# Performance work log

Hardware: AMD Instinct MI355X
Metric: run time of the kernel (lower is better)

## Reference

```python
import jax, jax.numpy as jnp
import numpy as np

N = 100000
E = 1600000
D_IN = 128
D_HID = 128
D_OUT = 64


def setup_inputs() -> dict:
    key = jax.random.key(0)
    ks = jax.random.split(key, 12)
    x = jax.random.normal(ks[0], (N, D_IN), dtype=jnp.float32)
    src = jax.random.randint(ks[1], (E,), 0, N, dtype=jnp.int32)
    dst = jax.random.randint(ks[2], (E,), 0, N, dtype=jnp.int32)
    def lin(k, din, dout):
        s = 1.0 / np.sqrt(din)
        return jax.random.uniform(k, (din, dout), jnp.float32, -s, s)
    return {
        "x": x, "src": src, "dst": dst,
        "Ws0": lin(ks[3], D_IN, D_HID), "Wn0": lin(ks[4], D_IN, D_HID), "b0": jnp.zeros((D_HID,), jnp.float32),
        "Ws1": lin(ks[5], D_HID, D_HID), "Wn1": lin(ks[6], D_HID, D_HID), "b1": jnp.zeros((D_HID,), jnp.float32),
        "Ws2": lin(ks[7], D_HID, D_OUT), "Wn2": lin(ks[8], D_HID, D_OUT), "b2": jnp.zeros((D_OUT,), jnp.float32),
    }


def _sage_conv(h, src, dst, Ws, Wn, b):
    # mean aggregation of neighbor (src) features onto dst nodes
    deg = jax.ops.segment_sum(jnp.ones((src.shape[0],), h.dtype), dst, num_segments=N)
    agg = jax.ops.segment_sum(h[src], dst, num_segments=N)  # [N, d_in]
    mean = agg / jnp.maximum(deg, 1.0)[:, None]
    return h @ Ws + mean @ Wn + b


def reference(x, src, dst, Ws0, Wn0, b0, Ws1, Wn1, b1, Ws2, Wn2, b2):
    h = _sage_conv(x, src, dst, Ws0, Wn0, b0)
    h = jax.nn.relu(h)  # dropout is identity in eval mode
    h = _sage_conv(h, src, dst, Ws1, Wn1, b1)
    h = jax.nn.relu(h)
    h = _sage_conv(h, src, dst, Ws2, Wn2, b2)
    return h
```

## Files before the change

### kernel.cpp

```cpp
#include <hip/hip_runtime.h>

#define NN 100000
#define NE 1600000
#define DF 128
#define TS 136
#define NCB 391
#define NWA 256
#define SZA 6250
#define NH (NCB * NWA)
#define CAPB 6144

typedef unsigned int uint32;
typedef unsigned short u16;
typedef _Float16 f16;
typedef f16 f16x8 __attribute__((ext_vector_type(8)));
typedef f16 f16x2 __attribute__((ext_vector_type(2)));
typedef float f32x4 __attribute__((ext_vector_type(4)));

__device__ __forceinline__ uint32 pk2(float a, float b) {
    union { f16x2 h; uint32 u; } v;
    v.h.x = (f16)a; v.h.y = (f16)b;
    return v.u;
}
__device__ __forceinline__ u16 f2h(float a) {
    union { f16 h; u16 u; } v; v.h = (f16)a; return v.u;
}


__global__ __launch_bounds__(256) void histA(const int* __restrict__ dst,
                                             int* __restrict__ H) {
    __shared__ int lh[NCB];
    int w = blockIdx.x, t = threadIdx.x;
    for (int i = t; i < NCB; i += 256) lh[i] = 0;
    __syncthreads();
    int e0 = w * SZA, e1 = min(e0 + SZA, NE);
    for (int e = e0 + t; e < e1; e += 256) atomicAdd(&lh[dst[e] >> 8], 1);
    __syncthreads();
    for (int i = t; i < NCB; i += 256) H[i * NWA + w] = lh[i];
}

__global__ __launch_bounds__(256) void sumCB(const int* __restrict__ H,
                                             int* __restrict__ CBT) {
    __shared__ int sm[256];
    int cb = blockIdx.x, t = threadIdx.x;
    sm[t] = H[cb * NWA + t];
    __syncthreads();
    for (int off = 128; off > 0; off >>= 1) {
        if (t < off) sm[t] += sm[t + off];
        __syncthreads();
    }
    if (t == 0) CBT[cb] = sm[0];
}

__global__ __launch_bounds__(512) void scanCBW(const int* __restrict__ CBT,
                                               const int* __restrict__ H,
                                               int* __restrict__ O,
                                               int* __restrict__ rowptr) {
    __shared__ int sm[512];
    __shared__ int sh[256];
    int cb = blockIdx.x, t = threadIdx.x;
    int v = (t < NCB) ? CBT[t] : 0;
    sm[t] = v;
    __syncthreads();
    for (int off = 1; off < 512; off <<= 1) {
        int x = (t >= off) ? sm[t - off] : 0;
        __syncthreads();
        sm[t] += x;
        __syncthreads();
    }
    if (cb == 0 && t == NCB - 1) {
        O[NH] = sm[t];
        rowptr[NN] = sm[t];
    }
    int cbo = sm[cb] - CBT[cb];
    int hv = (t < 256) ? H[cb * NWA + t] : 0;
    if (t < 256) sh[t] = hv;
    __syncthreads();
    for (int off = 1; off < 256; off <<= 1) {
        int x = (t >= off && t < 256) ? sh[t - off] : 0;
        __syncthreads();
        if (t < 256) sh[t] += x;
        __syncthreads();
    }
    if (t < 256) O[cb * NWA + t] = cbo + sh[t] - hv;
}

__global__ __launch_bounds__(1024) void passA(const int* __restrict__ src,
                                              const int* __restrict__ dst,
                                              const int* __restrict__ O,
                                              uint32* __restrict__ ebuf) {
    __shared__ int cur[NCB];
    int w = blockIdx.x, t = threadIdx.x;
    for (int i = t; i < NCB; i += 1024) cur[i] = O[i * NWA + w];
    __syncthreads();
    int e0 = w * SZA, e1 = min(e0 + SZA, NE);
    for (int e = e0 + t; e < e1; e += 1024) {
        int d = dst[e];
        int cb = d >> 8;
        int p = atomicAdd(&cur[cb], 1);
        ebuf[p] = ((uint32)src[e] << 8) | (uint32)(d & 255);
    }
}

__global__ __launch_bounds__(256) void passB(const uint32* __restrict__ ebuf,
                                             const int* __restrict__ O,
                                             int* __restrict__ rowptr,
                                             int* __restrict__ col) {
    __shared__ int hist[256], start[256], cur[256];
    __shared__ int seg[CAPB];
    int cb = blockIdx.x, t = threadIdx.x;
    int base = O[cb * NWA], end = O[(cb + 1) * NWA];
    int m = end - base;
    hist[t] = 0;
    __syncthreads();
    for (int i = t; i < m; i += 256) atomicAdd(&hist[ebuf[base + i] & 255], 1);
    __syncthreads();
    int v = hist[t];
    cur[t] = v;
    __syncthreads();
    for (int off = 1; off < 256; off <<= 1) {
        int x = (t >= off) ? cur[t - off] : 0;
        __syncthreads();
        cur[t] += x;
        __syncthreads();
    }
    start[t] = cur[t] - v;
    __syncthreads();
    int node = cb * 256 + t;
    if (node < NN) rowptr[node] = base + start[t];
    cur[t] = start[t];
    __syncthreads();
    if (m <= CAPB) {
        for (int i = t; i < m; i += 256) {
            uint32 u = ebuf[base + i];
            int p = atomicAdd(&cur[u & 255], 1);
            seg[p] = (int)(u >> 8);
        }
        __syncthreads();
        for (int i = t; i < m; i += 256) col[base + i] = seg[i];
    } else {
        for (int i = t; i < m; i += 256) {
            uint32 u = ebuf[base + i];
            int p = atomicAdd(&cur[u & 255], 1);
            col[base + p] = (int)(u >> 8);
        }
    }
}

__global__ void prep_cvt(const float* __restrict__ Ws0, const float* __restrict__ Wn0,
                         const float* __restrict__ Ws1, const float* __restrict__ Wn1,
                         const float* __restrict__ Ws2, const float* __restrict__ Wn2,
                         u16* __restrict__ WB,
                         const float* __restrict__ x, uint2* __restrict__ xh) {
    int b = blockIdx.x;
    if (b < 320) {
        int t = b * 256 + threadIdx.x;
        if (t < 65536) {
            int m = t >> 14;
            int local = t & 16383;
            int k = local >> 7, n = local & 127;
            const float* W = (m == 0) ? Ws0 : (m == 1) ? Wn0 : (m == 2) ? Ws1 : Wn1;
            WB[m * 16384 + n * 128 + k] = f2h(W[k * 128 + n]);
        } else {
            int local = t - 65536;
            int half = local >> 13;
            int idx = local & 8191;
            int k = idx >> 6, n = idx & 63;
            const float* W = half ? Wn2 : Ws2;
            WB[4 * 16384 + (n + half * 64) * 128 + k] = f2h(W[k * 64 + n]);
        }
    } else {
        int t = (b - 320) * 256 + threadIdx.x;
        if (t < NN * DF / 4) {
            float4 v = ((const float4*)x)[t];
            uint2 o;
            o.x = pk2(v.x, v.y);
            o.y = pk2(v.z, v.w);
            xh[t] = o;
        }
    }
}

__global__ __launch_bounds__(256) void gather_add_f16(const u16* __restrict__ gb,
                                                      const int* __restrict__ rowptr,
                                                      const int* __restrict__ col,
                                                      float* __restrict__ out) {
    int node = blockIdx.x * 32 + (threadIdx.x >> 3);
    int g = threadIdx.x & 7;
    int s = rowptr[node], e = rowptr[node + 1];
    float acc[8];
#pragma unroll
    for (int i = 0; i < 8; ++i) acc[i] = 0.f;
    int j = s;
    for (; j + 7 < e; j += 8) {
        int n0 = col[j],     n1 = col[j + 1], n2 = col[j + 2], n3 = col[j + 3];
        int n4 = col[j + 4], n5 = col[j + 5], n6 = col[j + 6], n7 = col[j + 7];
        f16x8 v0 = *(const f16x8*)(gb + (size_t)n0 * 64 + g * 8);
        f16x8 v1 = *(const f16x8*)(gb + (size_t)n1 * 64 + g * 8);
        f16x8 v2 = *(const f16x8*)(gb + (size_t)n2 * 64 + g * 8);
        f16x8 v3 = *(const f16x8*)(gb + (size_t)n3 * 64 + g * 8);
        f16x8 v4 = *(const f16x8*)(gb + (size_t)n4 * 64 + g * 8);
        f16x8 v5 = *(const f16x8*)(gb + (size_t)n5 * 64 + g * 8);
        f16x8 v6 = *(const f16x8*)(gb + (size_t)n6 * 64 + g * 8);
        f16x8 v7 = *(const f16x8*)(gb + (size_t)n7 * 64 + g * 8);
        f16x8 sA = (v0 + v1) + (v2 + v3);
        f16x8 sB = (v4 + v5) + (v6 + v7);
#pragma unroll
        for (int i = 0; i < 8; ++i) acc[i] += (float)sA[i] + (float)sB[i];
    }
    for (; j + 3 < e; j += 4) {
        int n0 = col[j], n1 = col[j + 1], n2 = col[j + 2], n3 = col[j + 3];
        f16x8 v0 = *(const f16x8*)(gb + (size_t)n0 * 64 + g * 8);
        f16x8 v1 = *(const f16x8*)(gb + (size_t)n1 * 64 + g * 8);
        f16x8 v2 = *(const f16x8*)(gb + (size_t)n2 * 64 + g * 8);
        f16x8 v3 = *(const f16x8*)(gb + (size_t)n3 * 64 + g * 8);
        f16x8 sv = (v0 + v1) + (v2 + v3);
#pragma unroll
        for (int i = 0; i < 8; ++i) acc[i] += (float)sv[i];
    }
    for (; j < e; ++j) {
        f16x8 v = *(const f16x8*)(gb + (size_t)col[j] * 64 + g * 8);
#pragma unroll
        for (int i = 0; i < 8; ++i) acc[i] += (float)v[i];
    }
    float invd = 1.f / fmaxf((float)(e - s), 1.f);
    float4* op = (float4*)(out + (size_t)node * 64 + g * 8);
    float4 a = op[0], b = op[1];
    a.x += acc[0] * invd; a.y += acc[1] * invd;
    a.z += acc[2] * invd; a.w += acc[3] * invd;
    b.x += acc[4] * invd; b.y += acc[5] * invd;
    b.z += acc[6] * invd; b.w += acc[7] * invd;
    op[0] = a; op[1] = b;
}

__device__ __forceinline__ void stage_a(u16* sm, const u16* g, int row0, int tid) {
#pragma unroll
    for (int i = 0; i < 8; ++i) {
        int idx = i * 256 + tid;
        int r = idx >> 4, c = (idx & 15) * 8;
        uint4 v = make_uint4(0, 0, 0, 0);
        int gr = row0 + r;
        if (gr < NN) v = *(const uint4*)(g + (size_t)gr * DF + c);
        *(uint4*)(sm + r * TS + c) = v;
    }
}

__device__ __forceinline__ void stage_w(u16* sm, const u16* wt, int nbase, int tid) {
#pragma unroll
    for (int i = 0; i < 4; ++i) {
        int idx = i * 256 + tid;
        int r = idx >> 4, c = (idx & 15) * 8;
        *(uint4*)(sm + r * TS + c) = *(const uint4*)(wt + (size_t)(nbase + r) * 128 + c);
    }
}

__device__ __forceinline__ f16x8 frag(const u16* sm, int row, int lane, int kc) {
    return *(const f16x8*)(sm + (row + (lane & 15)) * TS + kc * 32 + (lane >> 4) * 8);
}

__device__ __forceinline__ void mfma4(const u16* As, const u16* Bs, int wrow, int lane,
                                      f32x4 acc[2][8], int ab) {
    f16x8 a[2][4];
#pragma unroll
    for (int rt = 0; rt < 2; ++rt)
#pragma unroll
        for (int kc = 0; kc < 4; ++kc) a[rt][kc] = frag(As, wrow + rt * 16, lane, kc);
#pragma unroll
    for (int n = 0; n < 4; ++n) {
#pragma unroll
        for (int kc = 0; kc < 4; ++kc) {
            f16x8 b = frag(Bs, n * 16, lane, kc);
            acc[0][ab + n] = __builtin_amdgcn_mfma_f32_16x16x32_f16(a[0][kc], b, acc[0][ab + n], 0, 0, 0);
            acc[1][ab + n] = __builtin_amdgcn_mfma_f32_16x16x32_f16(a[1][kc], b, acc[1][ab + n], 0, 0, 0);
        }
    }
}

#define SW(WT, NB) { __syncthreads(); stage_w(Bs, WT, NB, tid); __syncthreads(); }

__device__ __forceinline__ void gather_As(u16* As, const u16* __restrict__ hb,
                                          const int* __restrict__ rowptr,
                                          const int* __restrict__ col,
                                          int row0, int tid) {
    int g = tid & 15;
    int rb = tid >> 4;
    const u16* hp = hb + g * 8;
#pragma unroll 1
    for (int p = 0; p < 8; ++p) {
        int r = p * 16 + rb;
        int gr = row0 + r;
        union { f16x8 h; uint4 u; } o;
        if (gr < NN) {
            int s = rowptr[gr], e = rowptr[gr + 1];
            float acc[8];
#pragma unroll
            for (int i = 0; i < 8; ++i) acc[i] = 0.f;
            int j = s;
            for (; j + 7 < e; j += 8) {
                int n0 = col[j],     n1 = col[j + 1], n2 = col[j + 2], n3 = col[j + 3];
                int n4 = col[j + 4], n5 = col[j + 5], n6 = col[j + 6], n7 = col[j + 7];
                f16x8 v0 = *(const f16x8*)(hp + (size_t)n0 * DF);
                f16x8 v1 = *(const f16x8*)(hp + (size_t)n1 * DF);
                f16x8 v2 = *(const f16x8*)(hp + (size_t)n2 * DF);
                f16x8 v3 = *(const f16x8*)(hp + (size_t)n3 * DF);
                f16x8 v4 = *(const f16x8*)(hp + (size_t)n4 * DF);
                f16x8 v5 = *(const f16x8*)(hp + (size_t)n5 * DF);
                f16x8 v6 = *(const f16x8*)(hp + (size_t)n6 * DF);
                f16x8 v7 = *(const f16x8*)(hp + (size_t)n7 * DF);
                f16x8 sA = (v0 + v1) + (v2 + v3);
                f16x8 sB = (v4 + v5) + (v6 + v7);
#pragma unroll
                for (int i = 0; i < 8; ++i) acc[i] += (float)sA[i] + (float)sB[i];
            }
            for (; j + 3 < e; j += 4) {
                int n0 = col[j], n1 = col[j + 1], n2 = col[j + 2], n3 = col[j + 3];
                f16x8 v0 = *(const f16x8*)(hp + (size_t)n0 * DF);
                f16x8 v1 = *(const f16x8*)(hp + (size_t)n1 * DF);
                f16x8 v2 = *(const f16x8*)(hp + (size_t)n2 * DF);
                f16x8 v3 = *(const f16x8*)(hp + (size_t)n3 * DF);
                f16x8 sv = (v0 + v1) + (v2 + v3);
#pragma unroll
                for (int i = 0; i < 8; ++i) acc[i] += (float)sv[i];
            }
            for (; j < e; ++j) {
                f16x8 v = *(const f16x8*)(hp + (size_t)col[j] * DF);
#pragma unroll
                for (int i = 0; i < 8; ++i) acc[i] += (float)v[i];
            }
            float invd = 1.f / fmaxf((float)(e - s), 1.f);
#pragma unroll
            for (int i = 0; i < 8; ++i) o.h[i] = (f16)(acc[i] * invd);
        } else {
            o.u = make_uint4(0, 0, 0, 0);
        }
        *(uint4*)(As + r * TS + g * 8) = o.u;
    }
}

__global__ __launch_bounds__(256) void fused_sage_f16(
    const u16* __restrict__ Hin,
    const u16* __restrict__ Ws, const u16* __restrict__ Wn,
    const float* __restrict__ bias,
    const int* __restrict__ rowptr, const int* __restrict__ col,
    u16* __restrict__ OutH) {
    __shared__ u16 As[128 * TS];
    __shared__ u16 Bs[64 * TS];
    const int tid = threadIdx.x;
    const int lane = tid & 63;
    const int wrow = (tid >> 6) * 32;
    const int row0 = blockIdx.x * 128;

    stage_w(Bs, Wn, 0, tid);
    gather_As(As, Hin, rowptr, col, row0, tid);
    __syncthreads();

    f32x4 acc[2][8];
#pragma unroll
    for (int rt = 0; rt < 2; ++rt)
#pragma unroll
        for (int n = 0; n < 8; ++n) acc[rt][n] = {0.f, 0.f, 0.f, 0.f};

    mfma4(As, Bs, wrow, lane, acc, 0);
    SW(Wn, 64); mfma4(As, Bs, wrow, lane, acc, 4);
    __syncthreads();
    stage_a(As, Hin, row0, tid);
    stage_w(Bs, Ws, 0, tid);
    __syncthreads();
    mfma4(As, Bs, wrow, lane, acc, 0);
    SW(Ws, 64); mfma4(As, Bs, wrow, lane, acc, 4);

    const int cit = lane & 15;
    const int rq = (lane >> 4) * 4;
#pragma unroll
    for (int rt = 0; rt < 2; ++rt)
#pragma unroll
        for (int n = 0; n < 8; ++n) {
            float bv = bias[n * 16 + cit];
            f32x4 v = acc[rt][n];
#pragma unroll
            for (int r = 0; r < 4; ++r) {
                int gr = row0 + wrow + rt * 16 + rq + r;
                if (gr < NN) {
                    float o = fmaxf(v[r] + bv, 0.f);
                    OutH[(size_t)gr * DF + n * 16 + cit] = f2h(o);
                }
            }
        }
}

__global__ __launch_bounds__(256) void gemm_l2_f16(
    const u16* __restrict__ H, const u16* __restrict__ W2,
    const float* __restrict__ b2, float* __restrict__ out, u16* __restrict__ g2) {
    __shared__ u16 As[128 * TS];
    __shared__ u16 Bs[64 * TS];
    const int tid = threadIdx.x;
    const int lane = tid & 63;
    const int wrow = (tid >> 6) * 32;
    const int row0 = blockIdx.x * 128;

    f32x4 acc[2][8];
#pragma unroll
    for (int rt = 0; rt < 2; ++rt)
#pragma unroll
        for (int n = 0; n < 8; ++n) acc[rt][n] = {0.f, 0.f, 0.f, 0.f};

    stage_a(As, H, row0, tid);
    stage_w(Bs, W2, 0, tid);
    __syncthreads();
    mfma4(As, Bs, wrow, lane, acc, 0);
    SW(W2, 64); mfma4(As, Bs, wrow, lane, acc, 4);

    const int cit = lane & 15;
    const int rq = (lane >> 4) * 4;
#pragma unroll
    for (int rt = 0; rt < 2; ++rt)
#pragma unroll
        for (int n = 0; n < 8; ++n) {
            f32x4 v = acc[rt][n];
            float bv = (n < 4) ? b2[n * 16 + cit] : 0.f;
#pragma unroll
            for (int r = 0; r < 4; ++r) {
                int gr = row0 + wrow + rt * 16 + rq + r;
                if (gr < NN) {
                    if (n < 4) out[(size_t)gr * 64 + n * 16 + cit] = v[r] + bv;
                    else g2[(size_t)gr * 64 + (n - 4) * 16 + cit] = f2h(v[r]);
                }
            }
        }
}

extern "C" void kernel_launch(void* const* d_in, const int* in_sizes, int n_in,
                              void* d_out, int out_size, void* d_ws, size_t ws_size,
                              hipStream_t stream) {
    const float* x   = (const float*)d_in[0];
    const int*   src = (const int*)d_in[1];
    const int*   dst = (const int*)d_in[2];
    const float* Ws0 = (const float*)d_in[3];
    const float* Wn0 = (const float*)d_in[4];
    const float* b0  = (const float*)d_in[5];
    const float* Ws1 = (const float*)d_in[6];
    const float* Wn1 = (const float*)d_in[7];
    const float* b1  = (const float*)d_in[8];
    const float* Ws2 = (const float*)d_in[9];
    const float* Wn2 = (const float*)d_in[10];
    const float* b2  = (const float*)d_in[11];
    float* out = (float*)d_out;

    int* H       = (int*)d_ws;
    int* O       = H + NH;
    int* CBT     = O + 100352;
    int* CBO     = CBT + 512;
    int* rowptr  = CBO + 512;
    int* col     = rowptr + 100352;
    uint32* ebuf = (uint32*)(col + NE);
    u16* WB      = (u16*)(ebuf + NE);
    u16* W0s = WB, *W0n = WB + 16384, *W1s = WB + 2 * 16384, *W1n = WB + 3 * 16384;
    u16* W2  = WB + 4 * 16384;
    u16* P1 = WB + 5 * 16384;
    u16* P3 = P1 + (size_t)NN * DF;

    const int gB = (NN + 127) / 128;

    histA<<<NWA, 256, 0, stream>>>(dst, H);
    sumCB<<<NCB, 256, 0, stream>>>(H, CBT);
    scanCBW<<<NCB, 512, 0, stream>>>(CBT, H, O, rowptr);
    passA<<<NWA, 1024, 0, stream>>>(src, dst, O, ebuf);
    passB<<<NCB, 256, 0, stream>>>(ebuf, O, rowptr, col);

    prep_cvt<<<320 + NN * DF / 4 / 256, 256, 0, stream>>>(
        Ws0, Wn0, Ws1, Wn1, Ws2, Wn2, WB, x, (uint2*)P1);

    fused_sage_f16<<<gB, 256, 0, stream>>>(P1, W0s, W0n, b0, rowptr, col, P3);

    fused_sage_f16<<<gB, 256, 0, stream>>>(P3, W1s, W1n, b1, rowptr, col, P1);

    gemm_l2_f16<<<gB, 256, 0, stream>>>(P1, W2, b2, out, P3);
    gather_add_f16<<<NN / 32, 256, 0, stream>>>(P3, rowptr, col, out);
}
```

Before: 428.6 us.

## Split fused gather+GEMM into standalone gather kernel and in-place GEMM

Moves neighbor mean aggregation for layers 0 and 1 out of the fused GEMM kernel into its own gather kernel. That kernel uses 8 threads per node and splits the feature dimension across two block panels, and it writes the mean to an intermediate buffer. The GEMM kernel then reads H and the mean and writes its output in place over H, staging the H tile before the mean tile. The goal is higher occupancy and memory-level parallelism for the irregular gathers, which were serialized inside the 128-row GEMM block with a large LDS footprint. The cost is an extra round trip through global memory for the mean and two more kernel launches. Writing the output in place over H is safe only because each block reads its own rows of H before writing them.

```diff
diff --git a/kernel.cpp b/kernel.cpp
--- a/kernel.cpp
+++ b/kernel.cpp
@@ -181,6 +181,58 @@
     }
 }
 
+__global__ __launch_bounds__(256) void gather_f16(const u16* __restrict__ hb,
+                                                  const int* __restrict__ rowptr,
+                                                  const int* __restrict__ col,
+                                                  u16* __restrict__ mean) {
+    int bid = blockIdx.x;
+    int panel = bid & 1;
+    int node = (bid >> 1) * 32 + (threadIdx.x >> 3);
+    int g = threadIdx.x & 7;
+    const u16* hp = hb + panel * 64 + g * 8;
+    int s = rowptr[node], e = rowptr[node + 1];
+    float acc[8];
+#pragma unroll
+    for (int i = 0; i < 8; ++i) acc[i] = 0.f;
+    int j = s;
+    for (; j + 7 < e; j += 8) {
+        int n0 = col[j],     n1 = col[j + 1], n2 = col[j + 2], n3 = col[j + 3];
+        int n4 = col[j + 4], n5 = col[j + 5], n6 = col[j + 6], n7 = col[j + 7];
+        f16x8 v0 = *(const f16x8*)(hp + (size_t)n0 * DF);
+        f16x8 v1 = *(const f16x8*)(hp + (size_t)n1 * DF);
+        f16x8 v2 = *(const f16x8*)(hp + (size_t)n2 * DF);
+        f16x8 v3 = *(const f16x8*)(hp + (size_t)n3 * DF);
+        f16x8 v4 = *(const f16x8*)(hp + (size_t)n4 * DF);
+        f16x8 v5 = *(const f16x8*)(hp + (size_t)n5 * DF);
+        f16x8 v6 = *(const f16x8*)(hp + (size_t)n6 * DF);
+        f16x8 v7 = *(const f16x8*)(hp + (size_t)n7 * DF);
+        f16x8 sA = (v0 + v1) + (v2 + v3);
+        f16x8 sB = (v4 + v5) + (v6 + v7);
+#pragma unroll
+        for (int i = 0; i < 8; ++i) acc[i] += (float)sA[i] + (float)sB[i];
+    }
+    for (; j + 3 < e; j += 4) {
+        int n0 = col[j], n1 = col[j + 1], n2 = col[j + 2], n3 = col[j + 3];
+        f16x8 v0 = *(const f16x8*)(hp + (size_t)n0 * DF);
+        f16x8 v1 = *(const f16x8*)(hp + (size_t)n1 * DF);
+        f16x8 v2 = *(const f16x8*)(hp + (size_t)n2 * DF);
+        f16x8 v3 = *(const f16x8*)(hp + (size_t)n3 * DF);
+        f16x8 sv = (v0 + v1) + (v2 + v3);
+#pragma unroll
+        for (int i = 0; i < 8; ++i) acc[i] += (float)sv[i];
+    }
+    for (; j < e; ++j) {
+        f16x8 v = *(const f16x8*)(hp + (size_t)col[j] * DF);
+#pragma unroll
+        for (int i = 0; i < 8; ++i) acc[i] += (float)v[i];
+    }
+    float invd = 1.f / fmaxf((float)(e - s), 1.f);
+    union { f16x8 h; uint4 u; } o;
+#pragma unroll
+    for (int i = 0; i < 8; ++i) o.h[i] = (f16)(acc[i] * invd);
+    *(uint4*)(mean + (size_t)node * DF + panel * 64 + g * 8) = o.u;
+}
+
 __global__ __launch_bounds__(256) void gather_add_f16(const u16* __restrict__ gb,
                                                       const int* __restrict__ rowptr,
                                                       const int* __restrict__ col,
@@ -278,71 +330,10 @@
 
 #define SW(WT, NB) { __syncthreads(); stage_w(Bs, WT, NB, tid); __syncthreads(); }
 
-__device__ __forceinline__ void gather_As(u16* As, const u16* __restrict__ hb,
-                                          const int* __restrict__ rowptr,
-                                          const int* __restrict__ col,
-                                          int row0, int tid) {
-    int g = tid & 15;
-    int rb = tid >> 4;
-    const u16* hp = hb + g * 8;
-#pragma unroll 1
-    for (int p = 0; p < 8; ++p) {
-        int r = p * 16 + rb;
-        int gr = row0 + r;
-        union { f16x8 h; uint4 u; } o;
-        if (gr < NN) {
-            int s = rowptr[gr], e = rowptr[gr + 1];
-            float acc[8];
-#pragma unroll
-            for (int i = 0; i < 8; ++i) acc[i] = 0.f;
-            int j = s;
-            for (; j + 7 < e; j += 8) {
-                int n0 = col[j],     n1 = col[j + 1], n2 = col[j + 2], n3 = col[j + 3];
-                int n4 = col[j + 4], n5 = col[j + 5], n6 = col[j + 6], n7 = col[j + 7];
-                f16x8 v0 = *(const f16x8*)(hp + (size_t)n0 * DF);
-                f16x8 v1 = *(const f16x8*)(hp + (size_t)n1 * DF);
-                f16x8 v2 = *(const f16x8*)(hp + (size_t)n2 * DF);
-                f16x8 v3 = *(const f16x8*)(hp + (size_t)n3 * DF);
-                f16x8 v4 = *(const f16x8*)(hp + (size_t)n4 * DF);
-                f16x8 v5 = *(const f16x8*)(hp + (size_t)n5 * DF);
-                f16x8 v6 = *(const f16x8*)(hp + (size_t)n6 * DF);
-                f16x8 v7 = *(const f16x8*)(hp + (size_t)n7 * DF);
-                f16x8 sA = (v0 + v1) + (v2 + v3);
-                f16x8 sB = (v4 + v5) + (v6 + v7);
-#pragma unroll
-                for (int i = 0; i < 8; ++i) acc[i] += (float)sA[i] + (float)sB[i];
-            }
-            for (; j + 3 < e; j += 4) {
-                int n0 = col[j], n1 = col[j + 1], n2 = col[j + 2], n3 = col[j + 3];
-                f16x8 v0 = *(const f16x8*)(hp + (size_t)n0 * DF);
-                f16x8 v1 = *(const f16x8*)(hp + (size_t)n1 * DF);
-                f16x8 v2 = *(const f16x8*)(hp + (size_t)n2 * DF);
-                f16x8 v3 = *(const f16x8*)(hp + (size_t)n3 * DF);
-                f16x8 sv = (v0 + v1) + (v2 + v3);
-#pragma unroll
-                for (int i = 0; i < 8; ++i) acc[i] += (float)sv[i];
-            }
-            for (; j < e; ++j) {
-                f16x8 v = *(const f16x8*)(hp + (size_t)col[j] * DF);
-#pragma unroll
-                for (int i = 0; i < 8; ++i) acc[i] += (float)v[i];
-            }
-            float invd = 1.f / fmaxf((float)(e - s), 1.f);
-#pragma unroll
-            for (int i = 0; i < 8; ++i) o.h[i] = (f16)(acc[i] * invd);
-        } else {
-            o.u = make_uint4(0, 0, 0, 0);
-        }
-        *(uint4*)(As + r * TS + g * 8) = o.u;
-    }
-}
-
-__global__ __launch_bounds__(256) void fused_sage_f16(
-    const u16* __restrict__ Hin,
+__global__ __launch_bounds__(256) void gemm_sage_f16(
+    const u16* H, const u16* M,
     const u16* __restrict__ Ws, const u16* __restrict__ Wn,
-    const float* __restrict__ bias,
-    const int* __restrict__ rowptr, const int* __restrict__ col,
-    u16* __restrict__ OutH) {
+    const float* __restrict__ bias, u16* OutH) {
     __shared__ u16 As[128 * TS];
     __shared__ u16 Bs[64 * TS];
     const int tid = threadIdx.x;
@@ -350,24 +341,23 @@
     const int wrow = (tid >> 6) * 32;
     const int row0 = blockIdx.x * 128;
 
+    f32x4 acc[2][8];
+#pragma unroll
+    for (int rt = 0; rt < 2; ++rt)
+#pragma unroll
+        for (int n = 0; n < 8; ++n) acc[rt][n] = {0.f, 0.f, 0.f, 0.f};
+
+    stage_a(As, H, row0, tid);
+    stage_w(Bs, Ws, 0, tid);
+    __syncthreads();
+    mfma4(As, Bs, wrow, lane, acc, 0);
+    SW(Ws, 64); mfma4(As, Bs, wrow, lane, acc, 4);
+    __syncthreads();
+    stage_a(As, M, row0, tid);
     stage_w(Bs, Wn, 0, tid);
-    gather_As(As, Hin, rowptr, col, row0, tid);
-    __syncthreads();
-
-    f32x4 acc[2][8];
-#pragma unroll
-    for (int rt = 0; rt < 2; ++rt)
-#pragma unroll
-        for (int n = 0; n < 8; ++n) acc[rt][n] = {0.f, 0.f, 0.f, 0.f};
-
+    __syncthreads();
     mfma4(As, Bs, wrow, lane, acc, 0);
     SW(Wn, 64); mfma4(As, Bs, wrow, lane, acc, 4);
-    __syncthreads();
-    stage_a(As, Hin, row0, tid);
-    stage_w(Bs, Ws, 0, tid);
-    __syncthreads();
-    mfma4(As, Bs, wrow, lane, acc, 0);
-    SW(Ws, 64); mfma4(As, Bs, wrow, lane, acc, 4);
 
     const int cit = lane & 15;
     const int rq = (lane >> 4) * 4;
@@ -470,9 +460,11 @@
     prep_cvt<<<320 + NN * DF / 4 / 256, 256, 0, stream>>>(
         Ws0, Wn0, Ws1, Wn1, Ws2, Wn2, WB, x, (uint2*)P1);
 
-    fused_sage_f16<<<gB, 256, 0, stream>>>(P1, W0s, W0n, b0, rowptr, col, P3);
-
-    fused_sage_f16<<<gB, 256, 0, stream>>>(P3, W1s, W1n, b1, rowptr, col, P1);
+    gather_f16<<<(NN / 32) * 2, 256, 0, stream>>>(P1, rowptr, col, P3);
+    gemm_sage_f16<<<gB, 256, 0, stream>>>(P1, P3, W0s, W0n, b0, P1);
+
+    gather_f16<<<(NN / 32) * 2, 256, 0, stream>>>(P1, rowptr, col, P3);
+    gemm_sage_f16<<<gB, 256, 0, stream>>>(P1, P3, W1s, W1n, b1, P1);
 
     gemm_l2_f16<<<gB, 256, 0, stream>>>(P1, W2, b2, out, P3);
     gather_add_f16<<<NN / 32, 256, 0, stream>>>(P3, rowptr, col, out);
```

Measured after the change: 382.6 us. 1.12x faster.
